# Optimization experiments

Measured on AMD Instinct MI355X. Metric: run time of the kernel, lower is better.

Reference implementation:

```python
import jax, jax.numpy as jnp
import numpy as np

N_EMBED = 4096
N_Q_HEADS = 32
N_KV_HEADS = 8
HEAD_DIM = N_EMBED // N_Q_HEADS  # 128
N_GROUPS = N_Q_HEADS // N_KV_HEADS  # 4
ROPE_BASE = 10000.0
BATCH, SEQ = 1, 2048


def setup_inputs() -> dict:
    key = jax.random.key(0)
    ks = jax.random.split(key, 5)
    hidden_state = jax.random.normal(ks[0], (BATCH, SEQ, N_EMBED), dtype=jnp.float32)
    # additive causal mask: 0 on/below diagonal, -inf above (SDPA float-mask semantics)
    causal = jnp.tril(jnp.ones((SEQ, SEQ), dtype=bool))
    attention_mask = jnp.where(causal, 0.0, -jnp.inf).astype(jnp.float32)[None, None]
    position_ids = jnp.arange(SEQ, dtype=jnp.int32)[None, :].repeat(BATCH, axis=0)
    s = 0.02
    Wq = jax.random.normal(ks[1], (N_EMBED, N_EMBED), dtype=jnp.float32) * s
    Wk = jax.random.normal(ks[2], (N_KV_HEADS * HEAD_DIM, N_EMBED), dtype=jnp.float32) * s
    Wv = jax.random.normal(ks[3], (N_KV_HEADS * HEAD_DIM, N_EMBED), dtype=jnp.float32) * s
    Wo = jax.random.normal(ks[4], (N_EMBED, N_EMBED), dtype=jnp.float32) * s
    return {"hidden_state": hidden_state, "attention_mask": attention_mask,
            "position_ids": position_ids, "Wq": Wq, "Wk": Wk, "Wv": Wv, "Wo": Wo}


def _rope_tables(position_ids):
    # mimic torch: inv_freq built in fp16 then used as float
    exponent = (jnp.arange(0, HEAD_DIM, 2, dtype=jnp.float16) / HEAD_DIM)
    inv_freq = (1.0 / (ROPE_BASE ** exponent)).astype(jnp.float32)  # [hd/2]
    m = position_ids.astype(jnp.float32)  # [bs, seq]
    m_theta = m[:, :, None] * inv_freq[None, None, :]  # [bs, seq, hd/2]
    m_theta = jnp.concatenate([m_theta, m_theta], axis=-1)  # [bs, seq, hd]
    return jnp.cos(m_theta), jnp.sin(m_theta)


def _rotate_half(x):
    half = x.shape[-1] // 2
    return jnp.concatenate([-x[..., half:], x[..., :half]], axis=-1)


def reference(hidden_state, attention_mask, position_ids, Wq, Wk, Wv, Wo):
    bs, seq, _ = hidden_state.shape
    q = (hidden_state @ Wq.T).reshape(bs, seq, N_Q_HEADS, HEAD_DIM).transpose(0, 2, 1, 3)
    k = (hidden_state @ Wk.T).reshape(bs, seq, N_KV_HEADS, HEAD_DIM).transpose(0, 2, 1, 3)
    v = (hidden_state @ Wv.T).reshape(bs, seq, N_KV_HEADS, HEAD_DIM).transpose(0, 2, 1, 3)

    cos, sin = _rope_tables(position_ids)
    cos, sin = cos[:, None], sin[:, None]  # broadcast over heads
    q = q * cos + _rotate_half(q) * sin
    k = k * cos + _rotate_half(k) * sin

    # GQA: group query heads per KV head instead of materializing KV copies
    qg = q.reshape(bs, N_KV_HEADS, N_GROUPS, seq, HEAD_DIM)
    scale = 1.0 / jnp.sqrt(jnp.float32(HEAD_DIM))
    scores = jnp.einsum('bhgqd,bhkd->bhgqk', qg, k) * scale + attention_mask[:, :, None]
    probs = jax.nn.softmax(scores, axis=-1)
    attn = jnp.einsum('bhgqk,bhkd->bhgqd', probs, v)  # [bs, kvh, g, seq, hd]
    attn = attn.reshape(bs, N_Q_HEADS, seq, HEAD_DIM).transpose(0, 2, 1, 3).reshape(bs, seq, N_EMBED)
    return attn @ Wo.T
```

## Files before the change

### kernel.cpp

```cpp
#include <hip/hip_runtime.h>
#include <hip/hip_bf16.h>

#define SEQ 2048
#define LDQKV 6144

typedef __attribute__((ext_vector_type(8))) __bf16 bf16x8;
typedef __attribute__((ext_vector_type(4))) __bf16 bf16x4;
typedef __attribute__((ext_vector_type(4))) float f32x4;

__device__ __forceinline__ void gload_lds16(const void* g, void* l) {
  __builtin_amdgcn_global_load_lds((__attribute__((address_space(1))) void*)(g),
                                   (__attribute__((address_space(3))) void*)(l), 16, 0, 0);
}

struct CvtArgs {
  const float* src0; const float* src1; const float* src2; const float* src3; const float* src4;
  __bf16* dst0; __bf16* dst1; __bf16* dst2; __bf16* dst3; __bf16* dst4;
};
__global__ __launch_bounds__(256) void cvt_all(CvtArgs a) {
  int b = blockIdx.x;
  const float* s; __bf16* d; int boff;
  if (b < 8192)       { s = a.src0; d = a.dst0; boff = b; }
  else if (b < 24576) { s = a.src1; d = a.dst1; boff = b - 8192; }
  else if (b < 28672) { s = a.src2; d = a.dst2; boff = b - 24576; }
  else if (b < 32768) { s = a.src3; d = a.dst3; boff = b - 28672; }
  else                { s = a.src4; d = a.dst4; boff = b - 32768; }
  long i = ((long)boff * 256 + threadIdx.x) * 4;
  f32x4 v = *(const f32x4*)(s + i);
  bf16x4 o;
  #pragma unroll
  for (int j = 0; j < 4; ++j) o[j] = (__bf16)v[j];
  *(bf16x4*)(d + i) = o;
}

__global__ __launch_bounds__(256) void rope_tab_k(const int* __restrict__ pos,
                                                  float* __restrict__ tab) {
  int i = blockIdx.x * 256 + threadIdx.x;
  int s = i >> 6, j = i & 63;
  float p = (float)pos[s];
  float pw = powf(10000.0f, (float)j * (1.0f / 64.0f));
  _Float16 ph = (_Float16)pw;
  _Float16 ivh = (_Float16)(1.0f / (float)ph);
  float freq = (float)ivh;
  float th = p * freq;
  tab[i] = cosf(th);
  tab[SEQ * 64 + i] = sinf(th);
}

__global__ __launch_bounds__(256) void rope_apply_k(__bf16* __restrict__ qkv,
                                                    const float* __restrict__ tab) {
  int i = blockIdx.x * 256 + threadIdx.x;
  int dc = i & 7;
  int ht = (i >> 3) % 40;
  int s = i / 320;
  long col = (ht < 32) ? (long)ht * 128 : (long)4096 + (long)(ht - 32) * 128;
  __bf16* p = qkv + (long)s * LDQKV + col + dc * 8;
  bf16x8 lo = *(bf16x8*)p;
  bf16x8 hi = *(bf16x8*)(p + 64);
  const float* tc = tab + (long)s * 64 + dc * 8;
  const float* ts = tc + SEQ * 64;
  bf16x8 lo2, hi2;
  #pragma unroll
  for (int e = 0; e < 8; ++e) {
    float c = tc[e], sn = ts[e];
    float lv = (float)lo[e], hv = (float)hi[e];
    lo2[e] = (__bf16)(lv * c - hv * sn);
    hi2[e] = (__bf16)(hv * c + lv * sn);
  }
  *(bf16x8*)p = lo2;
  *(bf16x8*)(p + 64) = hi2;
}

template<int BN, bool OUT_BF16>
__global__ __launch_bounds__(512, 2) void gemm8(const __bf16* __restrict__ A,
                                                const __bf16* __restrict__ B,
                                                void* __restrict__ C,
                                                int K, int ldc) {
  constexpr int BHR = BN / 2;
  constexpr int NFR = BN / 128;
  constexpr int LB  = BHR / 64;
  constexpr int NW  = 1 + LB;
  extern __shared__ __bf16 lds[];
  __bf16* Ab = lds;
  __bf16* Bb = lds + 16384;

  const int tid = threadIdx.x;
  const int wave = tid >> 6, lane = tid & 63;
  const int l15 = lane & 15, l4 = lane >> 4;
  const int wm = wave >> 2, wn = wave & 3;

  const int orig = blockIdx.x;
  const int swz = (orig & 7) * 32 + (orig >> 3);
  const int bx = swz & 15, by = swz >> 4;
  const long brow = (long)bx * 128, bcol = (long)by * BN;

  const int rS = tid >> 3;
  const int cS = ((tid & 7) * 8) ^ ((rS & 7) << 3);
  const int NT = K >> 6;

  auto stageA = [&](int buf, int qm, int t) {
    const __bf16* src = A + (brow + qm * 64 + rS) * (long)K + t * 64 + cS;
    gload_lds16(src, Ab + (buf * 2 + qm) * 4096 + wave * 512);
  };
  auto stageB = [&](int buf, int qn, int t) {
    #pragma unroll
    for (int i = 0; i < LB; ++i) {
      const __bf16* src = B + (bcol + qn * BHR + i * 64 + rS) * (long)K + t * 64 + cS;
      gload_lds16(src, Bb + (buf * 2 + qn) * (BHR * 64) + i * 4096 + wave * 512);
    }
  };

  bf16x8 afLo[2][2], afHi[2][2], b0[NFR][2], b1[NFR][2];
  auto readA = [&](bf16x8 (&dst)[2][2], int buf, int qm) {
    #pragma unroll
    for (int mi = 0; mi < 2; ++mi) {
      int r = wm * 32 + mi * 16 + l15;
      #pragma unroll
      for (int kf = 0; kf < 2; ++kf) {
        int c = (kf * 32 + l4 * 8) ^ ((r & 7) << 3);
        dst[mi][kf] = *(const bf16x8*)&Ab[(buf * 2 + qm) * 4096 + r * 64 + c];
      }
    }
  };
  auto readB = [&](bf16x8 (&dst)[NFR][2], int buf, int qn) {
    #pragma unroll
    for (int ni = 0; ni < NFR; ++ni) {
      int r = wn * (BN / 8) + ni * 16 + l15;
      #pragma unroll
      for (int kf = 0; kf < 2; ++kf) {
        int c = (kf * 32 + l4 * 8) ^ ((r & 7) << 3);
        dst[ni][kf] = *(const bf16x8*)&Bb[(buf * 2 + qn) * (BHR * 64) + r * 64 + c];
      }
    }
  };

  f32x4 acc[2][2][2][NFR] = {};
  auto mfmaQ = [&](bf16x8 (&af)[2][2], bf16x8 (&bf_)[NFR][2], f32x4 (&ac)[2][NFR]) {
    __builtin_amdgcn_s_setprio(1);
    #pragma unroll
    for (int mi = 0; mi < 2; ++mi)
      #pragma unroll
      for (int ni = 0; ni < NFR; ++ni)
        #pragma unroll
        for (int kf = 0; kf < 2; ++kf)
          ac[mi][ni] = __builtin_amdgcn_mfma_f32_16x16x32_bf16(af[mi][kf], bf_[ni][kf], ac[mi][ni], 0, 0, 0);
    __builtin_amdgcn_s_setprio(0);
  };

  #define VM_WAIT() do { \
    if constexpr (NW == 4) asm volatile("s_waitcnt vmcnt(4)" ::: "memory"); \
    else                   asm volatile("s_waitcnt vmcnt(3)" ::: "memory"); \
  } while (0)
  #define PH_BAR() do { __builtin_amdgcn_s_barrier(); __builtin_amdgcn_sched_barrier(0); } while (0)

  stageA(0, 0, 0); stageB(0, 0, 0); stageA(0, 1, 0); stageB(0, 1, 0);
  VM_WAIT();
  PH_BAR();

  for (int t = 0; t < NT; ++t) {
    const int buf = t & 1, nb = buf ^ 1;
    const bool pf = (t + 1 < NT);
    if (pf) stageA(nb, 0, t + 1);
    readA(afLo, buf, 0); readB(b0, buf, 0);
    mfmaQ(afLo, b0, acc[0][0]);
    VM_WAIT();
    PH_BAR();
    if (pf) stageB(nb, 0, t + 1);
    readA(afHi, buf, 1);
    mfmaQ(afHi, b0, acc[1][0]);
    VM_WAIT();
    PH_BAR();
    if (pf) stageA(nb, 1, t + 1);
    readB(b1, buf, 1);
    mfmaQ(afHi, b1, acc[1][1]);
    PH_BAR();
    if (pf) stageB(nb, 1, t + 1);
    mfmaQ(afLo, b1, acc[0][1]);
    VM_WAIT();
    PH_BAR();
  }
  #undef VM_WAIT
  #undef PH_BAR

  #pragma unroll
  for (int qm = 0; qm < 2; ++qm)
    #pragma unroll
    for (int qn = 0; qn < 2; ++qn)
      #pragma unroll
      for (int mi = 0; mi < 2; ++mi)
        #pragma unroll
        for (int ni = 0; ni < NFR; ++ni)
          #pragma unroll
          for (int j = 0; j < 4; ++j) {
            long rr = brow + qm * 64 + wm * 32 + mi * 16 + l4 * 4 + j;
            long cc = bcol + qn * BHR + wn * (BN / 8) + ni * 16 + l15;
            float v = acc[qm][qn][mi][ni][j];
            if (OUT_BF16) ((__bf16*)C)[rr * ldc + cc] = (__bf16)v;
            else          ((float*)C)[rr * ldc + cc] = v;
          }
}

__global__ __launch_bounds__(256) void flash_k(const __bf16* __restrict__ qkv,
                                               __bf16* __restrict__ ctx) {
  __shared__ __align__(16) __bf16 Kl[8192];
  __shared__ __align__(16) __bf16 Vt[8192];
  __shared__ __align__(16) __bf16 Pl[4][1024];

  const int bid = blockIdx.x;
  const int h = bid & 31;
  const int qt = 31 - (bid >> 5);
  const int kvh = h >> 2;
  const int q0 = qt * 64;
  const int tid = threadIdx.x, wave = tid >> 6, lane = tid & 63;
  const int l15 = lane & 15, l4 = lane >> 4;
  const int d2 = tid & 63, grp = tid >> 6;

  const __bf16* Qp = qkv + (long)h * 128;
  const __bf16* Kp = qkv + 4096 + (long)kvh * 128;
  const __bf16* Vp = qkv + 5120 + (long)kvh * 128;

  bf16x8 aq[4];
  {
    long qr = q0 + wave * 16 + l15;
    #pragma unroll
    for (int ks = 0; ks < 4; ++ks)
      aq[ks] = *(const bf16x8*)(Qp + qr * LDQKV + ks * 32 + l4 * 8);
  }
  f32x4 accO[8] = {};
  float lsum[4] = {0.f, 0.f, 0.f, 0.f};
  const float cexp = 0.08838834764831845f * 1.4426950408889634f;

  for (int kv0 = 0; kv0 <= q0; kv0 += 64) {
    __syncthreads();
    #pragma unroll
    for (int i = 0; i < 4; ++i) {
      int fo = i * 2048 + wave * 512 + lane * 8;
      int r = fo >> 7, c = fo & 127;
      int cs = c ^ ((r & 7) << 3);
      gload_lds16(Kp + (long)(kv0 + r) * LDQKV + cs, &Kl[i * 2048 + wave * 512]);
    }
    unsigned int vv[2][8];
    #pragma unroll
    for (int rep = 0; rep < 2; ++rep) {
      int cch = grp * 2 + rep;
      #pragma unroll
      for (int i = 0; i < 8; ++i)
        vv[rep][i] = *(const unsigned int*)(Vp + (long)(kv0 + cch * 8 + i) * LDQKV + 2 * d2);
    }
    #pragma unroll
    for (int rep = 0; rep < 2; ++rep) {
      int cch = grp * 2 + rep;
      #pragma unroll
      for (int half = 0; half < 2; ++half) {
        bf16x8 w;
        #pragma unroll
        for (int i = 0; i < 8; ++i)
          w[i] = __builtin_bit_cast(__bf16, (unsigned short)(vv[rep][i] >> (16 * half)));
        int d = 2 * d2 + half;
        *(bf16x8*)&Vt[d * 64 + ((cch * 8) ^ ((d2 & 7) * 8))] = w;
      }
    }
    __syncthreads();

    f32x4 s[4];
    #pragma unroll
    for (int t = 0; t < 4; ++t) s[t] = f32x4{0.f, 0.f, 0.f, 0.f};
    __builtin_amdgcn_s_setprio(1);
    #pragma unroll
    for (int t = 0; t < 4; ++t) {
      int r = t * 16 + l15;
      #pragma unroll
      for (int ks = 0; ks < 4; ++ks) {
        bf16x8 bk = *(const bf16x8*)&Kl[r * 128 + ((ks * 32 + l4 * 8) ^ ((r & 7) << 3))];
        s[t] = __builtin_amdgcn_mfma_f32_16x16x32_bf16(aq[ks], bk, s[t], 0, 0, 0);
      }
    }
    __builtin_amdgcn_s_setprio(0);

    const bool lastStep = (kv0 == q0);
    float pout[4][4];
    #pragma unroll
    for (int t = 0; t < 4; ++t)
      #pragma unroll
      for (int j = 0; j < 4; ++j) {
        float p = exp2f(s[t][j] * cexp);
        if (lastStep) {
          int qg = wave * 16 + l4 * 4 + j;
          int kg = t * 16 + l15;
          if (kg > qg) p = 0.f;
        }
        pout[t][j] = p;
      }
    #pragma unroll
    for (int j = 0; j < 4; ++j)
      lsum[j] += (pout[0][j] + pout[1][j]) + (pout[2][j] + pout[3][j]);

    #pragma unroll
    for (int t = 0; t < 4; ++t)
      #pragma unroll
      for (int j = 0; j < 4; ++j) {
        int r = l4 * 4 + j;
        int c = t * 16 + l15;
        Pl[wave][r * 64 + (c ^ ((r & 7) << 3))] = (__bf16)pout[t][j];
      }
    asm volatile("s_waitcnt lgkmcnt(0)" ::: "memory");
    __builtin_amdgcn_sched_barrier(0);
    bf16x8 ap[2];
    #pragma unroll
    for (int ks2 = 0; ks2 < 2; ++ks2) {
      int c = ks2 * 32 + l4 * 8;
      ap[ks2] = *(const bf16x8*)&Pl[wave][l15 * 64 + (c ^ ((l15 & 7) << 3))];
    }
    __builtin_amdgcn_s_setprio(1);
    #pragma unroll
    for (int dt = 0; dt < 8; ++dt) {
      int d = dt * 16 + l15;
      #pragma unroll
      for (int ks2 = 0; ks2 < 2; ++ks2) {
        int c = (ks2 * 32 + l4 * 8) ^ (((l15 >> 1) & 7) * 8);
        bf16x8 bv = *(const bf16x8*)&Vt[d * 64 + c];
        accO[dt] = __builtin_amdgcn_mfma_f32_16x16x32_bf16(ap[ks2], bv, accO[dt], 0, 0, 0);
      }
    }
    __builtin_amdgcn_s_setprio(0);
  }
  float rls[4];
  #pragma unroll
  for (int j = 0; j < 4; ++j) {
    float ls = lsum[j];
    ls += __shfl_xor(ls, 1, 16);
    ls += __shfl_xor(ls, 2, 16);
    ls += __shfl_xor(ls, 4, 16);
    ls += __shfl_xor(ls, 8, 16);
    rls[j] = 1.f / ls;
  }
  #pragma unroll
  for (int dt = 0; dt < 8; ++dt)
    #pragma unroll
    for (int j = 0; j < 4; ++j) {
      long qr = q0 + wave * 16 + l4 * 4 + j;
      long cc = (long)h * 128 + dt * 16 + l15;
      ctx[qr * 4096 + cc] = (__bf16)(accO[dt][j] * rls[j]);
    }
}

extern "C" void kernel_launch(void* const* d_in, const int* in_sizes, int n_in,
                              void* d_out, int out_size, void* d_ws, size_t ws_size,
                              hipStream_t stream) {
  const float* hs  = (const float*)d_in[0];
  const int*   pos = (const int*)d_in[2];
  const float* Wq  = (const float*)d_in[3];
  const float* Wk  = (const float*)d_in[4];
  const float* Wv  = (const float*)d_in[5];
  const float* Wo  = (const float*)d_in[6];
  char* ws = (char*)d_ws;
  __bf16* hsb  = (__bf16*)(ws + 0L);
  __bf16* wqkv = (__bf16*)(ws + 16777216L);
  __bf16* wob  = (__bf16*)(ws + 67108864L);
  __bf16* qkvb = (__bf16*)(ws + 100663296L);
  float*  tab  = (float*)(ws + 125829120L);
  __bf16* ctx  = (__bf16*)(ws + 126877696L);

  (void)hipFuncSetAttribute(reinterpret_cast<const void*>(&gemm8<384, true>),
                            hipFuncAttributeMaxDynamicSharedMemorySize, 131072);
  (void)hipFuncSetAttribute(reinterpret_cast<const void*>(&gemm8<256, false>),
                            hipFuncAttributeMaxDynamicSharedMemorySize, 98304);

  CvtArgs ca;
  ca.src0 = hs;  ca.dst0 = hsb;
  ca.src1 = Wq;  ca.dst1 = wqkv;
  ca.src2 = Wk;  ca.dst2 = wqkv + 16777216L;
  ca.src3 = Wv;  ca.dst3 = wqkv + 20971520L;
  ca.src4 = Wo;  ca.dst4 = wob;
  cvt_all<<<49152, 256, 0, stream>>>(ca);
  rope_tab_k<<<512, 256, 0, stream>>>(pos, tab);

  gemm8<384, true><<<256, 512, 131072, stream>>>(hsb, wqkv, qkvb, 4096, 6144);

  rope_apply_k<<<2560, 256, 0, stream>>>(qkvb, tab);

  flash_k<<<1024, 256, 0, stream>>>(qkvb, ctx);

  gemm8<256, false><<<256, 512, 98304, stream>>>(ctx, wob, d_out, 4096, 4096);
}
```

Measured before the change: 297.8 us.

## Shrink GEMM tiles to 4-wave blocks with doubled grid; widen cast kernel

Both GEMMs move from 512-thread blocks with 128x384 and 128x256 tiles to 256-thread blocks with 128x192 and 128x128 tiles, launching twice as many blocks. The staging loops, wave layout, swizzle and vmcnt waits are adjusted to match, and the last iteration now drains with vmcnt(0). The aim is more blocks per CU and better load balance across CUs. The cost is less data reuse per tile, so each block issues more global loads per MFMA. Separately, the fp32-to-bf16 cast kernel now handles 8 elements per thread with half the blocks.

```diff
diff --git a/kernel.cpp b/kernel.cpp
--- a/kernel.cpp
+++ b/kernel.cpp
@@ -20,17 +20,18 @@
 __global__ __launch_bounds__(256) void cvt_all(CvtArgs a) {
   int b = blockIdx.x;
   const float* s; __bf16* d; int boff;
-  if (b < 8192)       { s = a.src0; d = a.dst0; boff = b; }
-  else if (b < 24576) { s = a.src1; d = a.dst1; boff = b - 8192; }
-  else if (b < 28672) { s = a.src2; d = a.dst2; boff = b - 24576; }
-  else if (b < 32768) { s = a.src3; d = a.dst3; boff = b - 28672; }
-  else                { s = a.src4; d = a.dst4; boff = b - 32768; }
-  long i = ((long)boff * 256 + threadIdx.x) * 4;
-  f32x4 v = *(const f32x4*)(s + i);
-  bf16x4 o;
-  #pragma unroll
-  for (int j = 0; j < 4; ++j) o[j] = (__bf16)v[j];
-  *(bf16x4*)(d + i) = o;
+  if (b < 4096)       { s = a.src0; d = a.dst0; boff = b; }
+  else if (b < 12288) { s = a.src1; d = a.dst1; boff = b - 4096; }
+  else if (b < 14336) { s = a.src2; d = a.dst2; boff = b - 12288; }
+  else if (b < 16384) { s = a.src3; d = a.dst3; boff = b - 14336; }
+  else                { s = a.src4; d = a.dst4; boff = b - 16384; }
+  long i = ((long)boff * 256 + threadIdx.x) * 8;
+  f32x4 v0 = *(const f32x4*)(s + i);
+  f32x4 v1 = *(const f32x4*)(s + i + 4);
+  bf16x8 o;
+  #pragma unroll
+  for (int j = 0; j < 4; ++j) { o[j] = (__bf16)v0[j]; o[j + 4] = (__bf16)v1[j]; }
+  *(bf16x8*)(d + i) = o;
 }
 
 __global__ __launch_bounds__(256) void rope_tab_k(const int* __restrict__ pos,
@@ -72,14 +73,13 @@
 }
 
 template<int BN, bool OUT_BF16>
-__global__ __launch_bounds__(512, 2) void gemm8(const __bf16* __restrict__ A,
-                                                const __bf16* __restrict__ B,
-                                                void* __restrict__ C,
-                                                int K, int ldc) {
+__global__ __launch_bounds__(256, 2) void gemm2b(const __bf16* __restrict__ A,
+                                                 const __bf16* __restrict__ B,
+                                                 void* __restrict__ C,
+                                                 int K, int ldc) {
   constexpr int BHR = BN / 2;
-  constexpr int NFR = BN / 128;
-  constexpr int LB  = BHR / 64;
-  constexpr int NW  = 1 + LB;
+  constexpr int NFR = BHR / 32;
+  constexpr int LB  = BHR / 32;
   extern __shared__ __bf16 lds[];
   __bf16* Ab = lds;
   __bf16* Bb = lds + 16384;
@@ -87,10 +87,10 @@
   const int tid = threadIdx.x;
   const int wave = tid >> 6, lane = tid & 63;
   const int l15 = lane & 15, l4 = lane >> 4;
-  const int wm = wave >> 2, wn = wave & 3;
+  const int wm = wave >> 1, wn = wave & 1;
 
   const int orig = blockIdx.x;
-  const int swz = (orig & 7) * 32 + (orig >> 3);
+  const int swz = (orig & 7) * 64 + (orig >> 3);
   const int bx = swz & 15, by = swz >> 4;
   const long brow = (long)bx * 128, bcol = (long)by * BN;
 
@@ -99,14 +99,17 @@
   const int NT = K >> 6;
 
   auto stageA = [&](int buf, int qm, int t) {
-    const __bf16* src = A + (brow + qm * 64 + rS) * (long)K + t * 64 + cS;
-    gload_lds16(src, Ab + (buf * 2 + qm) * 4096 + wave * 512);
+    #pragma unroll
+    for (int i = 0; i < 2; ++i) {
+      const __bf16* src = A + (brow + qm * 64 + i * 32 + rS) * (long)K + t * 64 + cS;
+      gload_lds16(src, Ab + (buf * 2 + qm) * 4096 + i * 2048 + wave * 512);
+    }
   };
   auto stageB = [&](int buf, int qn, int t) {
     #pragma unroll
     for (int i = 0; i < LB; ++i) {
-      const __bf16* src = B + (bcol + qn * BHR + i * 64 + rS) * (long)K + t * 64 + cS;
-      gload_lds16(src, Bb + (buf * 2 + qn) * (BHR * 64) + i * 4096 + wave * 512);
+      const __bf16* src = B + (bcol + qn * BHR + i * 32 + rS) * (long)K + t * 64 + cS;
+      gload_lds16(src, Bb + (buf * 2 + qn) * (BHR * 64) + i * 2048 + wave * 512);
     }
   };
 
@@ -125,7 +128,7 @@
   auto readB = [&](bf16x8 (&dst)[NFR][2], int buf, int qn) {
     #pragma unroll
     for (int ni = 0; ni < NFR; ++ni) {
-      int r = wn * (BN / 8) + ni * 16 + l15;
+      int r = wn * (BHR / 2) + ni * 16 + l15;
       #pragma unroll
       for (int kf = 0; kf < 2; ++kf) {
         int c = (kf * 32 + l4 * 8) ^ ((r & 7) << 3);
@@ -147,14 +150,15 @@
     __builtin_amdgcn_s_setprio(0);
   };
 
-  #define VM_WAIT() do { \
-    if constexpr (NW == 4) asm volatile("s_waitcnt vmcnt(4)" ::: "memory"); \
-    else                   asm volatile("s_waitcnt vmcnt(3)" ::: "memory"); \
+  #define VM_WAIT(pf_) do { \
+    if (pf_) { if constexpr (LB == 3) asm volatile("s_waitcnt vmcnt(5)" ::: "memory"); \
+               else                   asm volatile("s_waitcnt vmcnt(4)" ::: "memory"); } \
+    else     asm volatile("s_waitcnt vmcnt(0)" ::: "memory"); \
   } while (0)
   #define PH_BAR() do { __builtin_amdgcn_s_barrier(); __builtin_amdgcn_sched_barrier(0); } while (0)
 
   stageA(0, 0, 0); stageB(0, 0, 0); stageA(0, 1, 0); stageB(0, 1, 0);
-  VM_WAIT();
+  VM_WAIT(true);
   PH_BAR();
 
   for (int t = 0; t < NT; ++t) {
@@ -163,12 +167,12 @@
     if (pf) stageA(nb, 0, t + 1);
     readA(afLo, buf, 0); readB(b0, buf, 0);
     mfmaQ(afLo, b0, acc[0][0]);
-    VM_WAIT();
+    VM_WAIT(pf);
     PH_BAR();
     if (pf) stageB(nb, 0, t + 1);
     readA(afHi, buf, 1);
     mfmaQ(afHi, b0, acc[1][0]);
-    VM_WAIT();
+    VM_WAIT(pf);
     PH_BAR();
     if (pf) stageA(nb, 1, t + 1);
     readB(b1, buf, 1);
@@ -176,7 +180,7 @@
     PH_BAR();
     if (pf) stageB(nb, 1, t + 1);
     mfmaQ(afLo, b1, acc[0][1]);
-    VM_WAIT();
+    VM_WAIT(pf);
     PH_BAR();
   }
   #undef VM_WAIT
@@ -193,7 +197,7 @@
           #pragma unroll
           for (int j = 0; j < 4; ++j) {
             long rr = brow + qm * 64 + wm * 32 + mi * 16 + l4 * 4 + j;
-            long cc = bcol + qn * BHR + wn * (BN / 8) + ni * 16 + l15;
+            long cc = bcol + qn * BHR + wn * (BHR / 2) + ni * 16 + l15;
             float v = acc[qm][qn][mi][ni][j];
             if (OUT_BF16) ((__bf16*)C)[rr * ldc + cc] = (__bf16)v;
             else          ((float*)C)[rr * ldc + cc] = v;
@@ -361,10 +365,10 @@
   float*  tab  = (float*)(ws + 125829120L);
   __bf16* ctx  = (__bf16*)(ws + 126877696L);
 
-  (void)hipFuncSetAttribute(reinterpret_cast<const void*>(&gemm8<384, true>),
-                            hipFuncAttributeMaxDynamicSharedMemorySize, 131072);
-  (void)hipFuncSetAttribute(reinterpret_cast<const void*>(&gemm8<256, false>),
-                            hipFuncAttributeMaxDynamicSharedMemorySize, 98304);
+  (void)hipFuncSetAttribute(reinterpret_cast<const void*>(&gemm2b<192, true>),
+                            hipFuncAttributeMaxDynamicSharedMemorySize, 81920);
+  (void)hipFuncSetAttribute(reinterpret_cast<const void*>(&gemm2b<128, false>),
+                            hipFuncAttributeMaxDynamicSharedMemorySize, 65536);
 
   CvtArgs ca;
   ca.src0 = hs;  ca.dst0 = hsb;
@@ -372,14 +376,14 @@
   ca.src2 = Wk;  ca.dst2 = wqkv + 16777216L;
   ca.src3 = Wv;  ca.dst3 = wqkv + 20971520L;
   ca.src4 = Wo;  ca.dst4 = wob;
-  cvt_all<<<49152, 256, 0, stream>>>(ca);
+  cvt_all<<<24576, 256, 0, stream>>>(ca);
   rope_tab_k<<<512, 256, 0, stream>>>(pos, tab);
 
-  gemm8<384, true><<<256, 512, 131072, stream>>>(hsb, wqkv, qkvb, 4096, 6144);
+  gemm2b<192, true><<<512, 256, 81920, stream>>>(hsb, wqkv, qkvb, 4096, 6144);
 
   rope_apply_k<<<2560, 256, 0, stream>>>(qkvb, tab);
 
   flash_k<<<1024, 256, 0, stream>>>(qkvb, ctx);
 
-  gemm8<256, false><<<256, 512, 98304, stream>>>(ctx, wob, d_out, 4096, 4096);
-}
+  gemm2b<128, false><<<512, 256, 65536, stream>>>(ctx, wob, d_out, 4096, 4096);
+}
```

After: 303.0 us. No clear change (+1.7%).
